# Kernel tuning notes

Hardware: AMD Instinct MI355X
Metric: run time of the kernel (lower is better)

Reference implementation:

```python
import jax, jax.numpy as jnp
import numpy as np

T, NINP, NSTATE, NCH, NLAYER, NCLASS = 8192, 128, 1024, 4, 3, 10
GH = NSTATE // NCH  # per-channel GRU hidden size
EPS = 1e-5


def setup_inputs() -> dict:
    key = jax.random.key(0)
    ks = jax.random.split(key, 32)
    rn = lambda k, shape, scale: (jax.random.normal(k, shape, jnp.float32) * scale)
    he = lambda k, shape: rn(k, shape, (2.0 / shape[-1]) ** 0.5)
    # log_s per layer/channel: scale = 10**i for channel i
    log_s = jnp.log(10.0 ** jnp.arange(NCH, dtype=jnp.float32))[None, :, None]
    inp = {
        "inputs": rn(ks[0], (T, NINP), 1.0),
        "h0": jnp.zeros((GH,), jnp.float32),
        "yinit_guess": jnp.zeros((T, GH), jnp.float32),
        # encoder MLP (ninp -> nstate -> nstate), he_uniform-like init, zero bias
        "enc_w1": he(ks[1], (NSTATE, NINP)),
        "enc_b1": jnp.zeros((NSTATE,), jnp.float32),
        "enc_w2": he(ks[2], (NSTATE, NSTATE)),
        "enc_b2": jnp.zeros((NSTATE,), jnp.float32),
        # per-layer, per-channel GRU params
        "gru_wih": rn(ks[3], (NLAYER, NCH, 3 * GH, NSTATE), NSTATE ** -0.5),  # lecun_normal
        "gru_whh": rn(ks[4], (NLAYER, NCH, 3 * GH, GH), GH ** -0.5),  # stand-in for orthogonal
        "gru_b": jnp.zeros((NLAYER, NCH, 3 * GH), jnp.float32),
        "gru_bn": jnp.zeros((NLAYER, NCH, GH), jnp.float32),
        "gru_log_s": jnp.broadcast_to(log_s, (NLAYER, NCH, 1)).astype(jnp.float32),
        # per-layer residual MLPs (nstate -> nstate -> nstate)
        "mlp_w1": he(ks[5], (NLAYER, NSTATE, NSTATE)),
        "mlp_b1": jnp.zeros((NLAYER, NSTATE), jnp.float32),
        "mlp_w2": he(ks[6], (NLAYER, NSTATE, NSTATE)),
        "mlp_b2": jnp.zeros((NLAYER, NSTATE), jnp.float32),
        # classifier MLP (nstate -> nstate -> nclass)
        "cls_w1": he(ks[7], (NSTATE, NSTATE)),
        "cls_b1": jnp.zeros((NSTATE,), jnp.float32),
        "cls_w2": he(ks[8], (NCLASS, NSTATE)),
        "cls_b2": jnp.zeros((NCLASS,), jnp.float32),
    }
    return inp


def layernorm(x):  # weightless/bias-less LayerNorm over last dim
    m = jnp.mean(x, axis=-1, keepdims=True)
    v = jnp.var(x, axis=-1, keepdims=True)
    return (x - m) / jnp.sqrt(v + EPS)


def mlp(x, w1, b1, w2, b2):  # eqx.nn.MLP depth=1, relu
    h = jax.nn.relu(x @ w1.T + b1)
    return h @ w2.T + b2


def scale_gru_channel(wih, whh, b, bn, log_s, x, h0):
    # ScaleGRU recurrence: per step hnew = GRU(x_t/s, h); h' = (hnew - h)/s + h.
    # This is the exact fixed point that seq1d (DEER) converges to; yinit_guess
    # only affects convergence speed, not the result.
    s = jnp.exp(jnp.clip(log_s, -10.0, 10.0))[0]
    ig = (x / s) @ wih.T + b  # [T, 3*GH], input gates precomputed (parallel GEMM)

    def step(h, ig_t):
        hg = whh @ h  # [3*GH]
        r = jax.nn.sigmoid(ig_t[:GH] + hg[:GH])
        z = jax.nn.sigmoid(ig_t[GH:2 * GH] + hg[GH:2 * GH])
        n = jnp.tanh(ig_t[2 * GH:] + r * (hg[2 * GH:] + bn))
        hnew = n + z * (h - n)  # equinox GRUCell output
        hout = (hnew - h) / s + h  # ScaleGRU rescaling
        return hout, hout

    _, ys = jax.lax.scan(step, h0, ig)
    return ys  # [T, GH]


def reference(inputs, h0, yinit_guess, enc_w1, enc_b1, enc_w2, enc_b2,
              gru_wih, gru_whh, gru_b, gru_bn, gru_log_s,
              mlp_w1, mlp_b1, mlp_w2, mlp_b2,
              cls_w1, cls_b1, cls_w2, cls_b2):
    del yinit_guess  # initial guess for the DEER solver; exact solution is independent of it
    x = mlp(inputs, enc_w1, enc_b1, enc_w2, enc_b2)  # encoder: [T, NSTATE]
    run_channels = jax.vmap(scale_gru_channel, in_axes=(0, 0, 0, 0, 0, None, None))
    for i in range(NLAYER):
        xi = layernorm(x)  # norms[i]
        ch = run_channels(gru_wih[i], gru_whh[i], gru_b[i], gru_bn[i],
                          gru_log_s[i], xi, h0)  # [NCH, T, GH]
        y = jnp.transpose(ch, (1, 0, 2)).reshape(T, NSTATE)  # concat channels on last dim
        y = layernorm(y + xi)  # norms[i+1]
        x = mlp(y, mlp_w1[i], mlp_b1[i], mlp_w2[i], mlp_b2[i]) + y
    return mlp(x, cls_w1, cls_b1, cls_w2, cls_b2)  # [T, NCLASS]
```

## Files before the change

kernel.cpp:

```cpp
#include <hip/hip_runtime.h>

#define T_SEQ  8192
#define NST    1024
#define GHH    256
#define LD_IG  3072
#define C_CH   512
#define NCHUNK 16
#define NDIAG  18

typedef _Float16 half8 __attribute__((ext_vector_type(8)));
typedef float f32x4 __attribute__((ext_vector_type(4)));

#define MFMA16(a, b, c) __builtin_amdgcn_mfma_f32_16x16x32_f16(a, b, c, 0, 0, 0)

__device__ __forceinline__ float sigmoid_f(float x) {
  return 1.0f / (1.0f + __expf(-x));
}
__device__ __forceinline__ float tanh_f(float x) {
  float ax = fabsf(x);
  float e = __expf(-2.0f * ax);
  float t = (1.0f - e) / (1.0f + e);
  return copysignf(t, x);
}

__device__ __forceinline__ const float* xin_ptr(const float* x0, const float* xn,
                                                int z, int c) {
  return (z == 0) ? x0 + (size_t)c * C_CH * NST
                  : xn + (size_t)(z - 1) * C_CH * NST;
}

__global__ __launch_bounds__(256) void prep_whh(const float* __restrict__ whh,
                                                half8* __restrict__ wB)
{
  const int idx = blockIdx.x * 256 + threadIdx.x;
  const int lc  = idx / 24576;
  const int rem = idx - lc * 24576;
  const int g_id = rem >> 6, l = rem & 63;
  const int nb = g_id >> 3, kc = g_id & 7;
  const int g = nb >> 4, ub = nb & 15;
  const int n = l & 15, kg = l >> 4;
  const int row = g * 256 + ub * 16 + n;
  const int col = kc * 32 + kg * 8;
  const float* src = whh + (size_t)lc * 196608 + (size_t)row * 256 + col;
  float4 x0 = *reinterpret_cast<const float4*>(src);
  float4 x1 = *reinterpret_cast<const float4*>(src + 4);
  half8 o;
  o[0] = (_Float16)x0.x; o[1] = (_Float16)x0.y;
  o[2] = (_Float16)x0.z; o[3] = (_Float16)x0.w;
  o[4] = (_Float16)x1.x; o[5] = (_Float16)x1.y;
  o[6] = (_Float16)x1.z; o[7] = (_Float16)x1.w;
  wB[idx] = o;
}

__global__ __launch_bounds__(256) void cvt_to_h(const float* __restrict__ src,
                                                _Float16* __restrict__ dst, int n8)
{
  const int i = blockIdx.x * 256 + threadIdx.x;
  if (i >= n8) return;
  float4 a = reinterpret_cast<const float4*>(src)[2 * i];
  float4 b = reinterpret_cast<const float4*>(src)[2 * i + 1];
  half8 o;
  o[0] = (_Float16)a.x; o[1] = (_Float16)a.y; o[2] = (_Float16)a.z; o[3] = (_Float16)a.w;
  o[4] = (_Float16)b.x; o[5] = (_Float16)b.y; o[6] = (_Float16)b.z; o[7] = (_Float16)b.w;
  reinterpret_cast<half8*>(dst)[i] = o;
}

template<int EPI, bool RELU>
__device__ __forceinline__ void gemm_body(
    const float* __restrict__ A, const _Float16* __restrict__ Wh,
    const float* __restrict__ bias, const float* __restrict__ R,
    float* __restrict__ C, int N, int K, const float* __restrict__ log_s,
    int bm, int bn, _Float16 (*As)[40], _Float16 (*Ws)[40])
{
  const int t = threadIdx.x;
  const int wave = t >> 6, l = t & 63;
  const int wm = (wave & 1) * 32, wn = (wave >> 1) * 32;
  const int sr = t >> 2, sc = (t & 3) * 8;
  const int fr = l & 15, fk = (l >> 4) * 8;

  f32x4 acc00 = {0.f, 0.f, 0.f, 0.f}, acc01 = acc00, acc10 = acc00, acc11 = acc00;

  const float* Ap     = A  + (size_t)(bm + sr) * K + sc;
  const _Float16* Wp  = Wh + (size_t)(bn + sr) * K + sc;

  for (int k0 = 0; k0 < K; k0 += 32) {
    float4 a0 = *reinterpret_cast<const float4*>(Ap + k0);
    float4 a1 = *reinterpret_cast<const float4*>(Ap + k0 + 4);
    half8 av;
    av[0] = (_Float16)a0.x; av[1] = (_Float16)a0.y;
    av[2] = (_Float16)a0.z; av[3] = (_Float16)a0.w;
    av[4] = (_Float16)a1.x; av[5] = (_Float16)a1.y;
    av[6] = (_Float16)a1.z; av[7] = (_Float16)a1.w;
    *reinterpret_cast<half8*>(&As[sr][sc]) = av;
    *reinterpret_cast<half8*>(&Ws[sr][sc]) =
        *reinterpret_cast<const half8*>(Wp + k0);
    __syncthreads();
    half8 af0 = *reinterpret_cast<const half8*>(&As[wm + fr][fk]);
    half8 af1 = *reinterpret_cast<const half8*>(&As[wm + 16 + fr][fk]);
    half8 bf0 = *reinterpret_cast<const half8*>(&Ws[wn + fr][fk]);
    half8 bf1 = *reinterpret_cast<const half8*>(&Ws[wn + 16 + fr][fk]);
    acc00 = MFMA16(af0, bf0, acc00);
    acc01 = MFMA16(af0, bf1, acc01);
    acc10 = MFMA16(af1, bf0, acc10);
    acc11 = MFMA16(af1, bf1, acc11);
    __syncthreads();
  }

#define EPI_STORE(ac, mi, ni) { \
    const int n_ = bn + wn + (ni) * 16 + fr; \
    const float bv = bias[n_]; \
    float sc_ = 1.f; \
    if (EPI == 1) { \
      float lsv = log_s[n_ / 768]; \
      lsv = fminf(fmaxf(lsv, -10.f), 10.f); \
      sc_ = __expf(-lsv); \
    } \
    _Pragma("unroll") \
    for (int q = 0; q < 4; ++q) { \
      const int m_ = bm + wm + (mi) * 16 + (l >> 4) * 4 + q; \
      float v = ac[q]; \
      if (EPI == 1) v *= sc_; \
      v += bv; \
      if (EPI == 2) v += R[(size_t)m_ * N + n_]; \
      if (RELU) v = fmaxf(v, 0.f); \
      C[(size_t)m_ * N + n_] = v; \
    } }
  EPI_STORE(acc00, 0, 0) EPI_STORE(acc01, 0, 1)
  EPI_STORE(acc10, 1, 0) EPI_STORE(acc11, 1, 1)
#undef EPI_STORE
}

template<int EPI, bool RELU>
__global__ __launch_bounds__(256) void gemm_h(
    const float* __restrict__ A, const _Float16* __restrict__ Wh,
    const float* __restrict__ bias, const float* __restrict__ R,
    float* __restrict__ C, int M, int N, int K,
    const float* __restrict__ log_s)
{
  __shared__ _Float16 As[64][40];
  __shared__ _Float16 Ws[64][40];
  gemm_body<EPI, RELU>(A, Wh, bias, R, C, N, K, log_s,
                       blockIdx.x * 64, blockIdx.y * 64, As, Ws);
}

template<int EPI, bool RELU>
__global__ __launch_bounds__(256) void gemm_b(
    const float* __restrict__ Abase, size_t Astride,
    const _Float16* __restrict__ Wbase, size_t Wstride,
    const float* __restrict__ bbase, size_t bstride,
    const float* __restrict__ Rbase, size_t Rstride,
    float* __restrict__ Cbase, size_t Cstride,
    int N, int K, const float* __restrict__ lsbase, int d)
{
  const int z = blockIdx.z;
  if ((unsigned)(d - z) >= NCHUNK) return;
  __shared__ _Float16 As[64][40];
  __shared__ _Float16 Ws[64][40];
  gemm_body<EPI, RELU>(Abase + (size_t)z * Astride, Wbase + (size_t)z * Wstride,
                       bbase + (size_t)z * bstride,
                       Rbase ? Rbase + (size_t)z * Rstride : nullptr,
                       Cbase + (size_t)z * Cstride, N, K,
                       lsbase ? lsbase + (size_t)z * 4 : nullptr,
                       blockIdx.x * 64, blockIdx.y * 64, As, Ws);
}

__global__ __launch_bounds__(256) void ln_pre_b(const float* __restrict__ x0,
                                                const float* __restrict__ xn,
                                                float* __restrict__ O, int d)
{
  const int z = blockIdx.x >> 9, row = blockIdx.x & 511;
  const int c = d - z;
  if ((unsigned)c >= NCHUNK) return;
  const int t = threadIdx.x;
  const float* X = xin_ptr(x0, xn, z, c) + (size_t)row * NST;
  float4 v = reinterpret_cast<const float4*>(X)[t];
  float s  = v.x + v.y + v.z + v.w;
  float ss = v.x * v.x + v.y * v.y + v.z * v.z + v.w * v.w;
#pragma unroll
  for (int m = 1; m < 64; m <<= 1) {
    s += __shfl_xor(s, m, 64); ss += __shfl_xor(ss, m, 64);
  }
  __shared__ float ps[4], pss[4];
  const int wv = t >> 6;
  if ((t & 63) == 0) { ps[wv] = s; pss[wv] = ss; }
  __syncthreads();
  s  = ps[0] + ps[1] + ps[2] + ps[3];
  ss = pss[0] + pss[1] + pss[2] + pss[3];
  const float mean = s * (1.f / 1024.f);
  const float var  = ss * (1.f / 1024.f) - mean * mean;
  const float rstd = rsqrtf(var + 1e-5f);
  v.x = (v.x - mean) * rstd; v.y = (v.y - mean) * rstd;
  v.z = (v.z - mean) * rstd; v.w = (v.w - mean) * rstd;
  reinterpret_cast<float4*>(O + ((size_t)z * C_CH + row) * NST)[t] = v;
}

__global__ __launch_bounds__(256) void ln2_b(float* __restrict__ Y,
                                             const float* __restrict__ x0,
                                             const float* __restrict__ xn,
                                             int d)
{
  const int z = blockIdx.x >> 9, row = blockIdx.x & 511;
  const int c = d - z;
  if ((unsigned)c >= NCHUNK) return;
  const int t = threadIdx.x;
  const int wv = t >> 6;
  __shared__ float ps[4], pss[4], ps2[4], pss2[4];

  const float* X = xin_ptr(x0, xn, z, c) + (size_t)row * NST;
  float* Yr = Y + ((size_t)z * C_CH + row) * NST;

  float4 xv = reinterpret_cast<const float4*>(X)[t];
  float s  = xv.x + xv.y + xv.z + xv.w;
  float ss = xv.x * xv.x + xv.y * xv.y + xv.z * xv.z + xv.w * xv.w;
#pragma unroll
  for (int m = 1; m < 64; m <<= 1) {
    s += __shfl_xor(s, m, 64); ss += __shfl_xor(ss, m, 64);
  }
  if ((t & 63) == 0) { ps[wv] = s; pss[wv] = ss; }
  __syncthreads();
  s = ps[0] + ps[1] + ps[2] + ps[3];
  ss = pss[0] + pss[1] + pss[2] + pss[3];
  float mean = s * (1.f / 1024.f);
  float var  = ss * (1.f / 1024.f) - mean * mean;
  float rstd = rsqrtf(var + 1e-5f);

  float4 yv = reinterpret_cast<const float4*>(Yr)[t];
  float4 v;
  v.x = yv.x + (xv.x - mean) * rstd;
  v.y = yv.y + (xv.y - mean) * rstd;
  v.z = yv.z + (xv.z - mean) * rstd;
  v.w = yv.w + (xv.w - mean) * rstd;

  s  = v.x + v.y + v.z + v.w;
  ss = v.x * v.x + v.y * v.y + v.z * v.z + v.w * v.w;
#pragma unroll
  for (int m = 1; m < 64; m <<= 1) {
    s += __shfl_xor(s, m, 64); ss += __shfl_xor(ss, m, 64);
  }
  if ((t & 63) == 0) { ps2[wv] = s; pss2[wv] = ss; }
  __syncthreads();
  s = ps2[0] + ps2[1] + ps2[2] + ps2[3];
  ss = pss2[0] + pss2[1] + pss2[2] + pss2[3];
  mean = s * (1.f / 1024.f);
  var  = ss * (1.f / 1024.f) - mean * mean;
  rstd = rsqrtf(var + 1e-5f);
  v.x = (v.x - mean) * rstd; v.y = (v.y - mean) * rstd;
  v.z = (v.z - mean) * rstd; v.w = (v.w - mean) * rstd;
  reinterpret_cast<float4*>(Yr)[t] = v;
}

#define SCAN_BAR() asm volatile("s_waitcnt lgkmcnt(0)\n\ts_barrier" ::: "memory")

#define DECLB(i) half8 B##i##_0, B##i##_1, B##i##_2, B##i##_3, \
                       B##i##_4, B##i##_5, B##i##_6, B##i##_7;
#define LOADBn(i, nb) \
  B##i##_0 = wpB[((nb)*8+0)*64]; B##i##_1 = wpB[((nb)*8+1)*64]; \
  B##i##_2 = wpB[((nb)*8+2)*64]; B##i##_3 = wpB[((nb)*8+3)*64]; \
  B##i##_4 = wpB[((nb)*8+4)*64]; B##i##_5 = wpB[((nb)*8+5)*64]; \
  B##i##_6 = wpB[((nb)*8+6)*64]; B##i##_7 = wpB[((nb)*8+7)*64];

#define KCSTEP(kc) { \
  half8 a = hp[(kc) * 4]; \
  a0 = MFMA16(a, B0_##kc, a0); a1 = MFMA16(a, B1_##kc, a1); \
  a2 = MFMA16(a, B2_##kc, a2); a3 = MFMA16(a, B3_##kc, a3); \
  a4 = MFMA16(a, B4_##kc, a4); a5 = MFMA16(a, B5_##kc, a5); }

__global__ __attribute__((amdgpu_flat_work_group_size(512, 512)))
void scan_diag(
    const half8* __restrict__ wB,
    const float* __restrict__ gbn,
    const float* __restrict__ gls,
    const float* __restrict__ igb,
    const float* __restrict__ h0,
    float* __restrict__ hst,
    float* __restrict__ yb,
    int d)
{
  const int lidx = blockIdx.x >> 2;
  const int ch   = blockIdx.x & 3;
  const int c    = d - lidx;
  if (c < 0 || c >= NCHUNK) return;

  const int j = threadIdx.x;
  const int w = j >> 6, l = j & 63;
  const int lc = lidx * 4 + ch;
  const float* igc = igb + (size_t)lidx * (C_CH * LD_IG) + ch * 768;
  float* yc        = yb + (size_t)lidx * (C_CH * NST) + ch * GHH;

  const half8* wpB = wB + (size_t)lc * 24576 + l;
  DECLB(0) DECLB(1) DECLB(2) DECLB(3) DECLB(4) DECLB(5)
  LOADBn(0, w)      LOADBn(1, w + 8)  LOADBn(2, w + 16)
  LOADBn(3, w + 24) LOADBn(4, w + 32) LOADBn(5, w + 40)

  __shared__ __align__(16) _Float16 hsl[2][GHH];

  const bool glane = (l < 32);
  const bool hi    = (l & 16) != 0;
  const int u = 16 * w + (l & 15) + (hi ? 128 : 0);

  float ls = gls[lc];
  ls = fminf(fmaxf(ls, -10.f), 10.f);
  const float inv_s = __expf(-ls);
  float bnu = 0.f, h = 0.f, ir = 0.f, iz = 0.f, in_ = 0.f;
  if (glane) {
    h   = (c == 0) ? h0[u] : hst[lc * GHH + u];
    bnu = gbn[lc * GHH + u];
    hsl[0][u] = (_Float16)h;
    ir = igc[u]; iz = igc[256 + u]; in_ = igc[512 + u];
  }
  SCAN_BAR();

  for (int t = 0; t < C_CH; ++t) {
    float nr = 0.f, nz = 0.f, nn = 0.f;
    if (glane && t + 1 < C_CH) {
      const float* p = igc + (size_t)(t + 1) * LD_IG;
      nr = p[u]; nz = p[256 + u]; nn = p[512 + u];
    }
    const half8* hp = reinterpret_cast<const half8*>(hsl[t & 1]) + (l >> 4);
    f32x4 a0 = {0.f, 0.f, 0.f, 0.f}, a1 = a0, a2 = a0, a3 = a0, a4 = a0, a5 = a0;
    KCSTEP(0) KCSTEP(1) KCSTEP(2) KCSTEP(3)
    KCSTEP(4) KCSTEP(5) KCSTEP(6) KCSTEP(7)
    if (glane) {
      const float pr = hi ? a1[0] : a0[0];
      const float pz = hi ? a3[0] : a2[0];
      const float pn = hi ? a5[0] : a4[0];
      const float rg = sigmoid_f(ir + pr);
      const float zg = sigmoid_f(iz + pz);
      const float ng = tanh_f(in_ + rg * (pn + bnu));
      const float hw = ng + zg * (h - ng);
      h = (hw - h) * inv_s + h;
      yc[(size_t)t * NST + u] = h;
      hsl[(t + 1) & 1][u] = (_Float16)h;
    }
    SCAN_BAR();
    ir = nr; iz = nz; in_ = nn;
  }
  if (glane) hst[lc * GHH + u] = h;
}

__global__ __launch_bounds__(256) void gemv_cls(const float* __restrict__ A,
                                                const float* __restrict__ W,
                                                const float* __restrict__ b,
                                                float* __restrict__ out)
{
  const int m = blockIdx.x, t = threadIdx.x;
  float4 a = reinterpret_cast<const float4*>(A + (size_t)m * NST)[t];
  float p[10];
#pragma unroll
  for (int n = 0; n < 10; ++n) {
    float4 w = reinterpret_cast<const float4*>(W + (size_t)n * NST)[t];
    p[n] = a.x * w.x + a.y * w.y + a.z * w.z + a.w * w.w;
  }
#pragma unroll
  for (int n = 0; n < 10; ++n)
#pragma unroll
    for (int msk = 1; msk < 64; msk <<= 1) p[n] += __shfl_xor(p[n], msk, 64);
  __shared__ float red[4][10];
  const int wv = t >> 6;
  if ((t & 63) == 0) {
#pragma unroll
    for (int n = 0; n < 10; ++n) red[wv][n] = p[n];
  }
  __syncthreads();
  if (t < 10) {
    float v = red[0][t] + red[1][t] + red[2][t] + red[3][t] + b[t];
    out[(size_t)m * 10 + t] = v;
  }
}

extern "C" void kernel_launch(void* const* d_in, const int* in_sizes, int n_in,
                              void* d_out, int out_size, void* d_ws, size_t ws_size,
                              hipStream_t stream) {
  const float* inputs = (const float*)d_in[0];
  const float* h0     = (const float*)d_in[1];
  const float* enc_w1 = (const float*)d_in[3];
  const float* enc_b1 = (const float*)d_in[4];
  const float* enc_w2 = (const float*)d_in[5];
  const float* enc_b2 = (const float*)d_in[6];
  const float* gwih   = (const float*)d_in[7];
  const float* gwhh   = (const float*)d_in[8];
  const float* gb     = (const float*)d_in[9];
  const float* gbn    = (const float*)d_in[10];
  const float* gls    = (const float*)d_in[11];
  const float* mw1    = (const float*)d_in[12];
  const float* mb1    = (const float*)d_in[13];
  const float* mw2    = (const float*)d_in[14];
  const float* mb2    = (const float*)d_in[15];
  const float* cw1    = (const float*)d_in[16];
  const float* cb1    = (const float*)d_in[17];
  const float* cw2    = (const float*)d_in[18];
  const float* cb2    = (const float*)d_in[19];
  float* out = (float*)d_out;

  char* ws = (char*)d_ws;
  float* x0    = (float*)(ws);
  float* xn    = (float*)(ws + 33554432ull);
  float* xitmp = (float*)(ws + 39845888ull);
  float* clsH  = xitmp;
  float* igbuf = (float*)(ws + 46137344ull);
  half8* gw16  = (half8*)(ws + 65011712ull);
  float* bufY  = (float*)(ws + 69730304ull);
  float* bufH  = (float*)(ws + 76021760ull);
  float* hst   = (float*)(ws + 82313216ull);
  _Float16* wf = (_Float16*)(ws + 82325504ull);
  float* encS  = (float*)(ws + 118239232ull);

  _Float16* wh_enc1 = wf;
  _Float16* wh_enc2 = wf + 131072;
  _Float16* wh_wih  = wf + 1179648;
  _Float16* wh_mw1  = wf + 10616832;
  _Float16* wh_mw2  = wf + 13762560;
  _Float16* wh_cw1  = wf + 16908288;

  const dim3 blk(256);
  const dim3 g_enc(8192 / 64, 1024 / 64);
  const dim3 g_ig_b(C_CH / 64, 3072 / 64, 3);
  const dim3 g_mlp_b(C_CH / 64, 1024 / 64, 3);
  const dim3 g_mlp(C_CH / 64, 1024 / 64);

  prep_whh<<<dim3(1152), blk, 0, stream>>>(gwhh, gw16);
  cvt_to_h<<<dim3(64),   blk, 0, stream>>>(enc_w1, wh_enc1, 16384);
  cvt_to_h<<<dim3(512),  blk, 0, stream>>>(enc_w2, wh_enc2, 131072);
  cvt_to_h<<<dim3(4608), blk, 0, stream>>>(gwih,   wh_wih,  1179648);
  cvt_to_h<<<dim3(1536), blk, 0, stream>>>(mw1,    wh_mw1,  393216);
  cvt_to_h<<<dim3(1536), blk, 0, stream>>>(mw2,    wh_mw2,  393216);
  cvt_to_h<<<dim3(512),  blk, 0, stream>>>(cw1,    wh_cw1,  131072);

  gemm_h<0, true ><<<g_enc, blk, 0, stream>>>(inputs, wh_enc1, enc_b1, nullptr,
                                              encS, 8192, 1024, 128, nullptr);
  gemm_h<0, false><<<g_enc, blk, 0, stream>>>(encS, wh_enc2, enc_b2, nullptr,
                                              x0, 8192, 1024, 1024, nullptr);

  for (int d = 0; d < NDIAG; ++d) {
    ln_pre_b<<<dim3(3 * C_CH), blk, 0, stream>>>(x0, xn, xitmp, d);
    gemm_b<1, false><<<g_ig_b, blk, 0, stream>>>(
        xitmp, (size_t)C_CH * NST, wh_wih, 3145728ull, gb, 3072ull,
        nullptr, 0ull, igbuf, (size_t)C_CH * LD_IG, 3072, 1024, gls, d);
    scan_diag<<<dim3(12), dim3(512), 0, stream>>>(gw16, gbn, gls, igbuf,
                                                  h0, hst, bufY, d);
    ln2_b<<<dim3(3 * C_CH), blk, 0, stream>>>(bufY, x0, xn, d);
    gemm_b<0, true ><<<g_mlp_b, blk, 0, stream>>>(
        bufY, (size_t)C_CH * NST, wh_mw1, 1048576ull, mb1, 1024ull,
        nullptr, 0ull, bufH, (size_t)C_CH * NST, 1024, 1024, nullptr, d);
    gemm_b<2, false><<<g_mlp_b, blk, 0, stream>>>(
        bufH, (size_t)C_CH * NST, wh_mw2, 1048576ull, mb2, 1024ull,
        bufY, (size_t)C_CH * NST, xn, (size_t)C_CH * NST, 1024, 1024, nullptr, d);
    const int c2 = d - 2;
    if (0 <= c2 && c2 < NCHUNK) {
      gemm_h<0, true><<<g_mlp, blk, 0, stream>>>(
          xn + 2ull * C_CH * NST, wh_cw1, cb1, nullptr, clsH, C_CH, 1024, 1024, nullptr);
      gemv_cls<<<dim3(C_CH), blk, 0, stream>>>(clsH, cw2, cb2,
                                               out + (size_t)c2 * C_CH * 10);
    }
  }
}
```

Baseline: 11.04 ms.

## Fuse classifier hidden GEMM into MLP1 launch and batch final classifier GEMV

The classifier's first GEMM for the chunk that finished the previous diagonal now runs as a fourth z-slice inside the MLP1 GEMM launch, so it shares that launch and fills more CUs instead of running as separate small serial kernels. Classifier hidden activations for all chunks are stored in a full-size buffer that reuses the encoder scratch space. The last chunk's hidden GEMM runs after the loop, followed by one GEMV over all 8192 rows. This removes per-diagonal launches and tail serialization, at the cost of a lagged chunk index and a larger buffer that must not overlap live data.

```diff
diff --git a/kernel.cpp b/kernel.cpp
--- a/kernel.cpp
+++ b/kernel.cpp
@@ -162,6 +162,30 @@
                        Cbase + (size_t)z * Cstride, N, K,
                        lsbase ? lsbase + (size_t)z * 4 : nullptr,
                        blockIdx.x * 64, blockIdx.y * 64, As, Ws);
+}
+
+__global__ __launch_bounds__(256) void gemm_mlp1_cls(
+    const float* __restrict__ bufY, const _Float16* __restrict__ mw1h,
+    const float* __restrict__ mb1h, float* __restrict__ bufH,
+    const float* __restrict__ xn2, const _Float16* __restrict__ cw1h,
+    const float* __restrict__ cb1h, float* __restrict__ clsF, int d)
+{
+  const int z = blockIdx.z;
+  __shared__ _Float16 As[64][40];
+  __shared__ _Float16 Ws[64][40];
+  if (z < 3) {
+    if ((unsigned)(d - z) >= NCHUNK) return;
+    gemm_body<0, true>(bufY + (size_t)z * C_CH * NST, mw1h + (size_t)z * 1048576,
+                       mb1h + (size_t)z * 1024, nullptr,
+                       bufH + (size_t)z * C_CH * NST, 1024, 1024, nullptr,
+                       blockIdx.x * 64, blockIdx.y * 64, As, Ws);
+  } else {
+    const int cc = d - 3;
+    if ((unsigned)cc >= NCHUNK) return;
+    gemm_body<0, true>(xn2, cw1h, cb1h, nullptr,
+                       clsF + (size_t)cc * C_CH * NST, 1024, 1024, nullptr,
+                       blockIdx.x * 64, blockIdx.y * 64, As, Ws);
+  }
 }
 
 __global__ __launch_bounds__(256) void ln_pre_b(const float* __restrict__ x0,
@@ -396,7 +420,6 @@
   float* x0    = (float*)(ws);
   float* xn    = (float*)(ws + 33554432ull);
   float* xitmp = (float*)(ws + 39845888ull);
-  float* clsH  = xitmp;
   float* igbuf = (float*)(ws + 46137344ull);
   half8* gw16  = (half8*)(ws + 65011712ull);
   float* bufY  = (float*)(ws + 69730304ull);
@@ -404,6 +427,7 @@
   float* hst   = (float*)(ws + 82313216ull);
   _Float16* wf = (_Float16*)(ws + 82325504ull);
   float* encS  = (float*)(ws + 118239232ull);
+  float* clsF  = encS;
 
   _Float16* wh_enc1 = wf;
   _Float16* wh_enc2 = wf + 131072;
@@ -416,6 +440,7 @@
   const dim3 g_enc(8192 / 64, 1024 / 64);
   const dim3 g_ig_b(C_CH / 64, 3072 / 64, 3);
   const dim3 g_mlp_b(C_CH / 64, 1024 / 64, 3);
+  const dim3 g_mlp1c(C_CH / 64, 1024 / 64, 4);
   const dim3 g_mlp(C_CH / 64, 1024 / 64);
 
   prep_whh<<<dim3(1152), blk, 0, stream>>>(gwhh, gw16);
@@ -439,18 +464,14 @@
     scan_diag<<<dim3(12), dim3(512), 0, stream>>>(gw16, gbn, gls, igbuf,
                                                   h0, hst, bufY, d);
     ln2_b<<<dim3(3 * C_CH), blk, 0, stream>>>(bufY, x0, xn, d);
-    gemm_b<0, true ><<<g_mlp_b, blk, 0, stream>>>(
-        bufY, (size_t)C_CH * NST, wh_mw1, 1048576ull, mb1, 1024ull,
-        nullptr, 0ull, bufH, (size_t)C_CH * NST, 1024, 1024, nullptr, d);
+    gemm_mlp1_cls<<<g_mlp1c, blk, 0, stream>>>(
+        bufY, wh_mw1, mb1, bufH, xn + 2ull * C_CH * NST, wh_cw1, cb1, clsF, d);
     gemm_b<2, false><<<g_mlp_b, blk, 0, stream>>>(
         bufH, (size_t)C_CH * NST, wh_mw2, 1048576ull, mb2, 1024ull,
         bufY, (size_t)C_CH * NST, xn, (size_t)C_CH * NST, 1024, 1024, nullptr, d);
-    const int c2 = d - 2;
-    if (0 <= c2 && c2 < NCHUNK) {
-      gemm_h<0, true><<<g_mlp, blk, 0, stream>>>(
-          xn + 2ull * C_CH * NST, wh_cw1, cb1, nullptr, clsH, C_CH, 1024, 1024, nullptr);
-      gemv_cls<<<dim3(C_CH), blk, 0, stream>>>(clsH, cw2, cb2,
-                                               out + (size_t)c2 * C_CH * 10);
-    }
-  }
-}
+  }
+  gemm_h<0, true><<<g_mlp, blk, 0, stream>>>(
+      xn + 2ull * C_CH * NST, wh_cw1, cb1, nullptr,
+      clsF + 15ull * C_CH * NST, C_CH, 1024, 1024, nullptr);
+  gemv_cls<<<dim3(8192), blk, 0, stream>>>(clsF, cw2, cb2, out);
+}
```

New measurement: 10.70 ms. -3.0%, faster.
